# Kernel optimization log

Measured on AMD Instinct MI355X. Metric: run time of the kernel, lower is better.

Reference implementation:

```python
import jax, jax.numpy as jnp
import numpy as np
from math import sqrt

B, P, D = 4, 2048, 1024
H, DK = 16, 64  # n_heads, d_keys


def setup_inputs() -> dict:
    key = jax.random.key(0)
    ks = jax.random.split(key, 6)
    s = 1.0 / sqrt(D)
    return {
        "target_embedding": jax.random.normal(ks[0], (B, P, D), dtype=jnp.float32),
        "Wq": jax.random.normal(ks[1], (D, H * DK), dtype=jnp.float32) * s,
        "bq": jnp.zeros((H * DK,), dtype=jnp.float32),
        "Wk": jax.random.normal(ks[2], (D, H * DK), dtype=jnp.float32) * s,
        "bk": jnp.zeros((H * DK,), dtype=jnp.float32),
        "Wv": jax.random.normal(ks[3], (D, H * DK), dtype=jnp.float32) * s,
        "bv": jnp.zeros((H * DK,), dtype=jnp.float32),
        "Wo": jax.random.normal(ks[4], (H * DK, D), dtype=jnp.float32) * s,
        "bo": jnp.zeros((D,), dtype=jnp.float32),
    }


def reference(target_embedding, Wq, bq, Wk, bk, Wv, bv, Wo, bo):
    x = target_embedding
    b, p, _ = x.shape
    # QKV projections -> [B, P, H, DK]
    q = (x @ Wq + bq).reshape(b, p, H, DK)
    k = (x @ Wk + bk).reshape(b, p, H, DK)
    v = (x @ Wv + bv).reshape(b, p, H, DK)
    scale = 1.0 / sqrt(DK)
    scores = jnp.einsum("bphd,bqhd->bhpq", q, k)  # [B, H, P, P]
    A = jax.nn.softmax(scale * scores, axis=-1)  # dropout is identity in eval
    rep = jnp.einsum("bhpq,bqhd->bphd", A, v).reshape(b, p, H * DK)
    return rep @ Wo + bo
```

## Files before the change

### kernel.cpp

```cpp
#include <hip/hip_runtime.h>

typedef __attribute__((ext_vector_type(8))) short short8;
typedef __attribute__((ext_vector_type(4))) short short4v;
typedef __attribute__((ext_vector_type(4))) float f32x4;
typedef __attribute__((ext_vector_type(4))) unsigned short ushort4v;
typedef __attribute__((ext_vector_type(2))) unsigned int uint2v;

#define GLOBAL_AS __attribute__((address_space(1)))
#define LDS_AS    __attribute__((address_space(3)))

__device__ __forceinline__ unsigned short f2bf(float f) {
    unsigned int u = __float_as_uint(f);
    u += 0x7fffu + ((u >> 16) & 1u);
    return (unsigned short)(u >> 16);
}

__device__ __forceinline__ unsigned int pack_rhu(float a, float b) {
    unsigned int ua = __float_as_uint(a) + 0x8000u;
    unsigned int ub = __float_as_uint(b) + 0x8000u;
    return __builtin_amdgcn_perm(ub, ua, 0x07060302u);
}

__device__ __forceinline__ short4v pack4_rhu(float p0, float p1, float p2, float p3) {
    uint2v uu;
    uu[0] = pack_rhu(p0, p1);
    uu[1] = pack_rhu(p2, p3);
    return __builtin_bit_cast(short4v, uu);
}

__device__ __forceinline__ float fexp2(float x) {
    return __builtin_amdgcn_exp2f(x);
}

__device__ __forceinline__ void async_cp16(void* lds, const void* g) {
    __builtin_amdgcn_global_load_lds((GLOBAL_AS unsigned int*)g,
                                     (LDS_AS unsigned int*)lds, 16, 0, 0);
}

#define SCL2E 0.18033688011112042591999058512524f

__global__ void convert_x_kernel(const float* __restrict__ X,
                                 unsigned short* __restrict__ Xb) {
    int i = (blockIdx.x * 256 + threadIdx.x) * 4;
    float4 v = *(const float4*)&X[i];
    ushort4v o;
    o.x = f2bf(v.x); o.y = f2bf(v.y); o.z = f2bf(v.z); o.w = f2bf(v.w);
    *(ushort4v*)&Xb[i] = o;
}

__global__ void transpose_w_kernel(const float* __restrict__ Wq,
                                   const float* __restrict__ Wk,
                                   const float* __restrict__ Wv,
                                   const float* __restrict__ Wo,
                                   unsigned short* __restrict__ Wts) {
    __shared__ float tile[32][33];
    const int z = blockIdx.z;
    const float* src = (z == 0) ? Wq : (z == 1) ? Wk : (z == 2) ? Wv : Wo;
    unsigned short* dst = Wts + z * 1048576;
    const int tx = threadIdx.x, ty = threadIdx.y;
    const int x0 = blockIdx.x * 32, y0 = blockIdx.y * 32;
#pragma unroll
    for (int i = 0; i < 32; i += 8)
        tile[ty + i][tx] = src[(y0 + ty + i) * 1024 + x0 + tx];
    __syncthreads();
#pragma unroll
    for (int i = 0; i < 32; i += 8)
        dst[(x0 + ty + i) * 1024 + y0 + tx] = f2bf(tile[tx][ty + i]);
}

__global__ void transpose_v_kernel(const unsigned short* __restrict__ V,
                                   unsigned short* __restrict__ Vt) {
    __shared__ unsigned short tile[32][33];
    const int bh = blockIdx.z;
    const int p0 = blockIdx.x * 32, d0 = blockIdx.y * 32;
    const unsigned short* src = V + bh * (2048 * 64);
    unsigned short* dst = Vt + bh * (2048 * 64);
    const int tx = threadIdx.x, ty = threadIdx.y;
#pragma unroll
    for (int i = 0; i < 32; i += 8)
        tile[ty + i][tx] = src[(p0 + ty + i) * 64 + d0 + tx];
    __syncthreads();
#pragma unroll
    for (int i = 0; i < 32; i += 8)
        dst[(d0 + ty + i) * 2048 + p0 + tx] = tile[tx][ty + i];
}

__device__ __forceinline__ void gemm_mainloop_128(
    const unsigned short* __restrict__ A, const unsigned short* __restrict__ Bt,
    int m0, int n0, unsigned short* As, unsigned short* Bs, f32x4 acc[4][4]) {
    const int tid = threadIdx.x;
    const int lane = tid & 63;
    const int wave = tid >> 6;
    const int wr = wave >> 1, wc = wave & 1;
    const int c = lane & 15, quad = lane >> 4;

#pragma unroll
    for (int mt = 0; mt < 4; ++mt)
#pragma unroll
        for (int nt = 0; nt < 4; ++nt)
            acc[mt][nt] = (f32x4)0.0f;

    for (int k0 = 0; k0 < 1024; k0 += 32) {
#pragma unroll
        for (int i = 0; i < 2; ++i) {
            int s = tid + 256 * i;
            int r = s >> 2, gp = s & 3;
            int g = gp ^ ((r >> 1) & 3);
            async_cp16(&As[s * 8], &A[(m0 + r) * 1024 + k0 + g * 8]);
        }
#pragma unroll
        for (int i = 0; i < 2; ++i) {
            int s = tid + 256 * i;
            int r = s >> 2, gp = s & 3;
            int g = gp ^ ((r >> 1) & 3);
            async_cp16(&Bs[s * 8], &Bt[(n0 + r) * 1024 + k0 + g * 8]);
        }
        asm volatile("s_waitcnt vmcnt(0)" ::: "memory");
        __syncthreads();

        short8 af[4], bf[4];
#pragma unroll
        for (int mt = 0; mt < 4; ++mt) {
            int r = wr * 64 + mt * 16 + c;
            int gp = quad ^ ((r >> 1) & 3);
            af[mt] = *(const short8*)&As[r * 32 + gp * 8];
        }
#pragma unroll
        for (int nt = 0; nt < 4; ++nt) {
            int r = wc * 64 + nt * 16 + c;
            int gp = quad ^ ((r >> 1) & 3);
            bf[nt] = *(const short8*)&Bs[r * 32 + gp * 8];
        }
#pragma unroll
        for (int mt = 0; mt < 4; ++mt)
#pragma unroll
            for (int nt = 0; nt < 4; ++nt)
                acc[mt][nt] = __builtin_amdgcn_mfma_f32_16x16x32_bf16(
                    af[mt], bf[nt], acc[mt][nt], 0, 0, 0);
        __syncthreads();
    }
}

__global__ __launch_bounds__(256, 3) void gemm_qkv_kernel(
    const unsigned short* __restrict__ Xb, const unsigned short* __restrict__ Wts,
    const float* __restrict__ bq, const float* __restrict__ bk,
    const float* __restrict__ bv, unsigned short* __restrict__ Qb,
    unsigned short* __restrict__ Kb, unsigned short* __restrict__ Vb) {
    __shared__ __align__(16) unsigned short As[128 * 32];
    __shared__ __align__(16) unsigned short Bs[128 * 32];
    const int z = blockIdx.z;
    const unsigned short* Bt = Wts + z * 1048576;
    const float* bias = (z == 0) ? bq : (z == 1) ? bk : bv;
    const int m0 = blockIdx.y * 128, n0 = blockIdx.x * 128;
    f32x4 acc[4][4];
    gemm_mainloop_128(Xb, Bt, m0, n0, As, Bs, acc);

    const int lane = threadIdx.x & 63, wave = threadIdx.x >> 6;
    const int wr = wave >> 1, wc = wave & 1;
    const int c = lane & 15, quad = lane >> 4;
    unsigned short* dst = (z == 0) ? Qb : (z == 1) ? Kb : Vb;
    const float qscale = (z == 0) ? SCL2E : 1.0f;
#pragma unroll
    for (int nt = 0; nt < 4; ++nt) {
        int col = n0 + wc * 64 + nt * 16 + c;
        float bb = bias[col];
        int h = col >> 6, dk = col & 63;
#pragma unroll
        for (int mt = 0; mt < 4; ++mt) {
#pragma unroll
            for (int r = 0; r < 4; ++r) {
                int row = m0 + wr * 64 + mt * 16 + quad * 4 + r;
                int b = row >> 11, p = row & 2047;
                float v = (acc[mt][nt][r] + bb) * qscale;
                dst[((b * 16 + h) * 2048 + p) * 64 + dk] = f2bf(v);
            }
        }
    }
}

__device__ __forceinline__ void load_kv_regs(
    const unsigned short* __restrict__ Kbh, const unsigned short* __restrict__ Vbh,
    int k0, int tid, short8 kr[2], short8 vr[2]) {
#pragma unroll
    for (int i = 0; i < 2; ++i) {
        int s = tid + 256 * i;
        int r = s >> 3, gp = s & 7;
        int g = gp ^ (r & 7);
        kr[i] = *(const short8*)&Kbh[(k0 + r) * 64 + g * 8];
        vr[i] = *(const short8*)&Vbh[r * 2048 + k0 + g * 8];
    }
}

__global__ __launch_bounds__(256, 2) void attn_kernel(
    const unsigned short* __restrict__ Q, const unsigned short* __restrict__ K,
    const unsigned short* __restrict__ Vt, unsigned short* __restrict__ rep) {
    __shared__ __align__(16) unsigned short SMEM[16384];
    const int tid = threadIdx.x, lane = tid & 63, wave = tid >> 6;
    const int c = lane & 15, quad = lane >> 4;
    const int bh = blockIdx.y;
    const int q0 = blockIdx.x * 256 + wave * 64;
    const unsigned short* Qbh = Q + bh * (2048 * 64);
    const unsigned short* Kbh = K + bh * (2048 * 64);
    const unsigned short* Vbh = Vt + bh * (64 * 2048);

    short8 qf[4][2];
#pragma unroll
    for (int t = 0; t < 4; ++t)
#pragma unroll
        for (int ks = 0; ks < 2; ++ks)
            qf[t][ks] = *(const short8*)&Qbh[(q0 + t * 16 + c) * 64 + ks * 32 + quad * 8];

    short8 kr[2], vr[2];
    load_kv_regs(Kbh, Vbh, 0, tid, kr, vr);

    f32x4 o[4][4];
    float lpart[4] = {0.0f, 0.0f, 0.0f, 0.0f};
#pragma unroll
    for (int t = 0; t < 4; ++t)
#pragma unroll
        for (int d = 0; d < 4; ++d) o[t][d] = (f32x4)0.0f;

    for (int it = 0; it < 32; ++it) {
        const int buf = it & 1;
        unsigned short* Ksb = &SMEM[buf * 4096];
        unsigned short* Vsb = &SMEM[8192 + buf * 4096];
#pragma unroll
        for (int i = 0; i < 2; ++i) {
            int s = tid + 256 * i;
            *(short8*)&Ksb[s * 8] = kr[i];
            *(short8*)&Vsb[s * 8] = vr[i];
        }
        __syncthreads();
        if (it < 31)
            load_kv_regs(Kbh, Vbh, (it + 1) * 64, tid, kr, vr);

        short8 kf[4][2];
#pragma unroll
        for (int nt = 0; nt < 4; ++nt)
#pragma unroll
            for (int ks = 0; ks < 2; ++ks) {
                int r = nt * 16 + c;
                int gp2 = (quad + 4 * ks) ^ (r & 7);
                kf[nt][ks] = *(const short8*)&Ksb[r * 64 + gp2 * 8];
            }

        short4v pfrag[4][4];
#pragma unroll
        for (int t = 0; t < 4; ++t) {
#pragma unroll
            for (int nt = 0; nt < 4; ++nt) {
                f32x4 z4 = (f32x4)0.0f;
                z4 = __builtin_amdgcn_mfma_f32_16x16x32_bf16(kf[nt][0], qf[t][0], z4, 0, 0, 0);
                z4 = __builtin_amdgcn_mfma_f32_16x16x32_bf16(kf[nt][1], qf[t][1], z4, 0, 0, 0);
                float p0 = fexp2(z4[0]), p1 = fexp2(z4[1]);
                float p2 = fexp2(z4[2]), p3 = fexp2(z4[3]);
                lpart[t] += (p0 + p1) + (p2 + p3);
                pfrag[nt][t] = pack4_rhu(p0, p1, p2, p3);
            }
        }

#pragma unroll
        for (int dkt = 0; dkt < 4; ++dkt) {
            int r = dkt * 16 + c;
#pragma unroll
            for (int kt = 0; kt < 4; ++kt) {
                int gbase = 2 * kt + (quad >> 1);
                int g = gbase ^ (r & 7);
                int eloff = g * 8 + (quad & 1) * 4;
                short4v vf4 = *(const short4v*)&Vsb[r * 64 + eloff];
#pragma unroll
                for (int t = 0; t < 4; ++t)
                    o[t][dkt] = __builtin_amdgcn_mfma_f32_16x16x16bf16_1k(
                        vf4, pfrag[kt][t], o[t][dkt], 0, 0, 0);
            }
        }
    }

    float inv[4];
#pragma unroll
    for (int t = 0; t < 4; ++t) {
        float l = lpart[t];
        l += __shfl_xor(l, 16);
        l += __shfl_xor(l, 32);
        inv[t] = 1.0f / l;
    }

    __syncthreads();
    const int b = bh >> 4, h = bh & 15;
    unsigned short* ob = &SMEM[wave * 2304];
#pragma unroll
    for (int pass = 0; pass < 2; ++pass) {
#pragma unroll
        for (int th = 0; th < 2; ++th) {
            int t = pass * 2 + th;
#pragma unroll
            for (int dkt = 0; dkt < 4; ++dkt) {
                short4v frag = pack4_rhu(o[t][dkt][0] * inv[t], o[t][dkt][1] * inv[t],
                                         o[t][dkt][2] * inv[t], o[t][dkt][3] * inv[t]);
                *(short4v*)&ob[(th * 16 + c) * 72 + dkt * 16 + quad * 4] = frag;
            }
        }
        asm volatile("s_waitcnt lgkmcnt(0)" ::: "memory");
#pragma unroll
        for (int sp = 0; sp < 4; ++sp) {
            int qr = sp * 8 + (lane >> 3);
            int d8 = (lane & 7) * 8;
            short8 row = *(const short8*)&ob[qr * 72 + d8];
            *(short8*)&rep[(b * 2048 + q0 + pass * 32 + qr) * 1024 + h * 64 + d8] = row;
        }
    }
}

__global__ __launch_bounds__(256, 3) void gemm_out_kernel(
    const unsigned short* __restrict__ rep, const unsigned short* __restrict__ Wot,
    const float* __restrict__ bo, float* __restrict__ out) {
    __shared__ __align__(16) unsigned short As[128 * 32];
    __shared__ __align__(16) unsigned short Bs[128 * 32];
    const int m0 = blockIdx.y * 128, n0 = blockIdx.x * 128;
    f32x4 acc[4][4];
    gemm_mainloop_128(rep, Wot, m0, n0, As, Bs, acc);
    const int lane = threadIdx.x & 63, wave = threadIdx.x >> 6;
    const int wr = wave >> 1, wc = wave & 1;
    const int c = lane & 15, quad = lane >> 4;
#pragma unroll
    for (int nt = 0; nt < 4; ++nt) {
        int col = n0 + wc * 64 + nt * 16 + c;
        float bb = bo[col];
#pragma unroll
        for (int mt = 0; mt < 4; ++mt) {
            int row = m0 + wr * 64 + mt * 16 + quad * 4;
#pragma unroll
            for (int r = 0; r < 4; ++r)
                out[(row + r) * 1024 + col] = acc[mt][nt][r] + bb;
        }
    }
}

extern "C" void kernel_launch(void* const* d_in, const int* in_sizes, int n_in,
                              void* d_out, int out_size, void* d_ws, size_t ws_size,
                              hipStream_t stream) {
    (void)in_sizes; (void)n_in; (void)out_size; (void)ws_size;
    const float* X  = (const float*)d_in[0];
    const float* Wq = (const float*)d_in[1];
    const float* bq = (const float*)d_in[2];
    const float* Wk = (const float*)d_in[3];
    const float* bk = (const float*)d_in[4];
    const float* Wv = (const float*)d_in[5];
    const float* bv = (const float*)d_in[6];
    const float* Wo = (const float*)d_in[7];
    const float* bo = (const float*)d_in[8];
    float* out = (float*)d_out;

    char* ws = (char*)d_ws;
    unsigned short* Xb   = (unsigned short*)(ws);
    unsigned short* Wts  = (unsigned short*)(ws + (16u << 20));
    unsigned short* Qb   = (unsigned short*)(ws + (24u << 20));
    unsigned short* Kb   = (unsigned short*)(ws + (40u << 20));
    unsigned short* Vb   = (unsigned short*)(ws + (56u << 20));
    unsigned short* Vtb  = (unsigned short*)(ws);
    unsigned short* repb = (unsigned short*)(ws + (56u << 20));

    convert_x_kernel<<<8192, 256, 0, stream>>>(X, Xb);
    transpose_w_kernel<<<dim3(32, 32, 4), dim3(32, 8), 0, stream>>>(Wq, Wk, Wv, Wo, Wts);
    gemm_qkv_kernel<<<dim3(8, 64, 3), 256, 0, stream>>>(Xb, Wts, bq, bk, bv, Qb, Kb, Vb);
    transpose_v_kernel<<<dim3(64, 2, 64), dim3(32, 8), 0, stream>>>(Vb, Vtb);
    attn_kernel<<<dim3(8, 64), 256, 0, stream>>>(Qb, Kb, Vtb, repb);
    gemm_out_kernel<<<dim3(8, 64), 256, 0, stream>>>(repb, Wts + 3 * 1048576, bo, out);
}
```

Before: 310.0 us.

## Fuse prep kernels, write V transposed from QKV GEMM, read K/V directly in attention

Merges the X conversion and weight transpose into one launch. The QKV GEMM epilogue now stages V through shared memory and writes it already transposed, which removes the separate V transpose kernel. The attention kernel drops its LDS double-buffered K/V staging and block barriers and loads fragments straight from global memory (relying on L2), with a remapped block index that groups heads. Direct global loads avoid barrier cost but may raise memory latency and duplicate traffic across waves.

Result: slower. 383.2 us (+23.6%).

```diff
diff --git a/kernel.cpp b/kernel.cpp
--- a/kernel.cpp
+++ b/kernel.cpp
@@ -39,50 +39,40 @@
 
 #define SCL2E 0.18033688011112042591999058512524f
 
-__global__ void convert_x_kernel(const float* __restrict__ X,
-                                 unsigned short* __restrict__ Xb) {
-    int i = (blockIdx.x * 256 + threadIdx.x) * 4;
-    float4 v = *(const float4*)&X[i];
-    ushort4v o;
-    o.x = f2bf(v.x); o.y = f2bf(v.y); o.z = f2bf(v.z); o.w = f2bf(v.w);
-    *(ushort4v*)&Xb[i] = o;
-}
-
-__global__ void transpose_w_kernel(const float* __restrict__ Wq,
-                                   const float* __restrict__ Wk,
-                                   const float* __restrict__ Wv,
-                                   const float* __restrict__ Wo,
-                                   unsigned short* __restrict__ Wts) {
-    __shared__ float tile[32][33];
+__global__ void prep_kernel(const float* __restrict__ X,
+                            const float* __restrict__ Wq,
+                            const float* __restrict__ Wk,
+                            const float* __restrict__ Wv,
+                            const float* __restrict__ Wo,
+                            unsigned short* __restrict__ Xb,
+                            unsigned short* __restrict__ Wts) {
     const int z = blockIdx.z;
-    const float* src = (z == 0) ? Wq : (z == 1) ? Wk : (z == 2) ? Wv : Wo;
-    unsigned short* dst = Wts + z * 1048576;
-    const int tx = threadIdx.x, ty = threadIdx.y;
-    const int x0 = blockIdx.x * 32, y0 = blockIdx.y * 32;
-#pragma unroll
-    for (int i = 0; i < 32; i += 8)
-        tile[ty + i][tx] = src[(y0 + ty + i) * 1024 + x0 + tx];
-    __syncthreads();
-#pragma unroll
-    for (int i = 0; i < 32; i += 8)
-        dst[(x0 + ty + i) * 1024 + y0 + tx] = f2bf(tile[tx][ty + i]);
-}
-
-__global__ void transpose_v_kernel(const unsigned short* __restrict__ V,
-                                   unsigned short* __restrict__ Vt) {
-    __shared__ unsigned short tile[32][33];
-    const int bh = blockIdx.z;
-    const int p0 = blockIdx.x * 32, d0 = blockIdx.y * 32;
-    const unsigned short* src = V + bh * (2048 * 64);
-    unsigned short* dst = Vt + bh * (2048 * 64);
-    const int tx = threadIdx.x, ty = threadIdx.y;
-#pragma unroll
-    for (int i = 0; i < 32; i += 8)
-        tile[ty + i][tx] = src[(p0 + ty + i) * 64 + d0 + tx];
-    __syncthreads();
-#pragma unroll
-    for (int i = 0; i < 32; i += 8)
-        dst[(d0 + ty + i) * 2048 + p0 + tx] = tile[tx][ty + i];
+    if (z < 4) {
+        __shared__ float tile[32][33];
+        const float* src = (z == 0) ? Wq : (z == 1) ? Wk : (z == 2) ? Wv : Wo;
+        unsigned short* dst = Wts + z * 1048576;
+        const int tx = threadIdx.x, ty = threadIdx.y;
+        const int x0 = blockIdx.x * 32, y0 = blockIdx.y * 32;
+#pragma unroll
+        for (int i = 0; i < 32; i += 8)
+            tile[ty + i][tx] = src[(y0 + ty + i) * 1024 + x0 + tx];
+        __syncthreads();
+#pragma unroll
+        for (int i = 0; i < 32; i += 8)
+            dst[(x0 + ty + i) * 1024 + y0 + tx] = f2bf(tile[tx][ty + i]);
+    } else {
+        const int tid = threadIdx.y * 32 + threadIdx.x;
+        const int chunk = blockIdx.y * 32 + blockIdx.x;
+        const int base = chunk * 8192;
+#pragma unroll
+        for (int pass = 0; pass < 8; ++pass) {
+            int i = base + pass * 1024 + tid * 4;
+            float4 v = *(const float4*)&X[i];
+            ushort4v o;
+            o.x = f2bf(v.x); o.y = f2bf(v.y); o.z = f2bf(v.z); o.w = f2bf(v.w);
+            *(ushort4v*)&Xb[i] = o;
+        }
+    }
 }
 
 __device__ __forceinline__ void gemm_mainloop_128(
@@ -145,9 +135,10 @@
     const unsigned short* __restrict__ Xb, const unsigned short* __restrict__ Wts,
     const float* __restrict__ bq, const float* __restrict__ bk,
     const float* __restrict__ bv, unsigned short* __restrict__ Qb,
-    unsigned short* __restrict__ Kb, unsigned short* __restrict__ Vb) {
-    __shared__ __align__(16) unsigned short As[128 * 32];
-    __shared__ __align__(16) unsigned short Bs[128 * 32];
+    unsigned short* __restrict__ Kb, unsigned short* __restrict__ Vtb) {
+    __shared__ __align__(16) unsigned short SH[17408];
+    unsigned short* As = SH;
+    unsigned short* Bs = SH + 4096;
     const int z = blockIdx.z;
     const unsigned short* Bt = Wts + z * 1048576;
     const float* bias = (z == 0) ? bq : (z == 1) ? bk : bv;
@@ -155,50 +146,66 @@
     f32x4 acc[4][4];
     gemm_mainloop_128(Xb, Bt, m0, n0, As, Bs, acc);
 
-    const int lane = threadIdx.x & 63, wave = threadIdx.x >> 6;
+    const int tid = threadIdx.x;
+    const int lane = tid & 63, wave = tid >> 6;
     const int wr = wave >> 1, wc = wave & 1;
     const int c = lane & 15, quad = lane >> 4;
-    unsigned short* dst = (z == 0) ? Qb : (z == 1) ? Kb : Vb;
-    const float qscale = (z == 0) ? SCL2E : 1.0f;
-#pragma unroll
-    for (int nt = 0; nt < 4; ++nt) {
-        int col = n0 + wc * 64 + nt * 16 + c;
-        float bb = bias[col];
-        int h = col >> 6, dk = col & 63;
-#pragma unroll
-        for (int mt = 0; mt < 4; ++mt) {
-#pragma unroll
-            for (int r = 0; r < 4; ++r) {
-                int row = m0 + wr * 64 + mt * 16 + quad * 4 + r;
-                int b = row >> 11, p = row & 2047;
-                float v = (acc[mt][nt][r] + bb) * qscale;
-                dst[((b * 16 + h) * 2048 + p) * 64 + dk] = f2bf(v);
-            }
-        }
-    }
-}
-
-__device__ __forceinline__ void load_kv_regs(
-    const unsigned short* __restrict__ Kbh, const unsigned short* __restrict__ Vbh,
-    int k0, int tid, short8 kr[2], short8 vr[2]) {
-#pragma unroll
-    for (int i = 0; i < 2; ++i) {
-        int s = tid + 256 * i;
-        int r = s >> 3, gp = s & 7;
-        int g = gp ^ (r & 7);
-        kr[i] = *(const short8*)&Kbh[(k0 + r) * 64 + g * 8];
-        vr[i] = *(const short8*)&Vbh[r * 2048 + k0 + g * 8];
+    const int b = m0 >> 11, p0 = m0 & 2047;
+
+    if (z < 2) {
+        unsigned short* dst = (z == 0) ? Qb : Kb;
+        const float qscale = (z == 0) ? SCL2E : 1.0f;
+#pragma unroll
+        for (int nt = 0; nt < 4; ++nt) {
+            int col = n0 + wc * 64 + nt * 16 + c;
+            float bb = bias[col];
+            int h = col >> 6, dk = col & 63;
+#pragma unroll
+            for (int mt = 0; mt < 4; ++mt) {
+#pragma unroll
+                for (int r = 0; r < 4; ++r) {
+                    int p = p0 + wr * 64 + mt * 16 + quad * 4 + r;
+                    float v = (acc[mt][nt][r] + bb) * qscale;
+                    dst[((b * 16 + h) * 2048 + p) * 64 + dk] = f2bf(v);
+                }
+            }
+        }
+    } else {
+#pragma unroll
+        for (int nt = 0; nt < 4; ++nt) {
+            int col = wc * 64 + nt * 16 + c;
+            float bb = bias[n0 + col];
+#pragma unroll
+            for (int mt = 0; mt < 4; ++mt) {
+                int p = wr * 64 + mt * 16 + quad * 4;
+                short4v v = pack4_rhu(acc[mt][nt][0] + bb, acc[mt][nt][1] + bb,
+                                      acc[mt][nt][2] + bb, acc[mt][nt][3] + bb);
+                *(short4v*)&SH[col * 136 + p] = v;
+            }
+        }
+        __syncthreads();
+#pragma unroll
+        for (int pass = 0; pass < 8; ++pass) {
+            int col = pass * 16 + (tid >> 4);
+            int gcol = n0 + col;
+            int h = gcol >> 6, dk = gcol & 63;
+            int p8 = (tid & 15) * 8;
+            short8 row = *(const short8*)&SH[col * 136 + p8];
+            *(short8*)&Vtb[((b * 16 + h) * 64 + dk) * 2048 + p0 + p8] = row;
+        }
     }
 }
 
 __global__ __launch_bounds__(256, 2) void attn_kernel(
     const unsigned short* __restrict__ Q, const unsigned short* __restrict__ K,
     const unsigned short* __restrict__ Vt, unsigned short* __restrict__ rep) {
-    __shared__ __align__(16) unsigned short SMEM[16384];
+    __shared__ __align__(16) unsigned short ob[4][2304];
     const int tid = threadIdx.x, lane = tid & 63, wave = tid >> 6;
     const int c = lane & 15, quad = lane >> 4;
-    const int bh = blockIdx.y;
-    const int q0 = blockIdx.x * 256 + wave * 64;
+    const int id = blockIdx.x;
+    const int bh = (id & 7) * 8 + ((id >> 3) & 7);
+    const int qblk = id >> 6;
+    const int q0 = qblk * 256 + wave * 64;
     const unsigned short* Qbh = Q + bh * (2048 * 64);
     const unsigned short* Kbh = K + bh * (2048 * 64);
     const unsigned short* Vbh = Vt + bh * (64 * 2048);
@@ -210,9 +217,6 @@
         for (int ks = 0; ks < 2; ++ks)
             qf[t][ks] = *(const short8*)&Qbh[(q0 + t * 16 + c) * 64 + ks * 32 + quad * 8];
 
-    short8 kr[2], vr[2];
-    load_kv_regs(Kbh, Vbh, 0, tid, kr, vr);
-
     f32x4 o[4][4];
     float lpart[4] = {0.0f, 0.0f, 0.0f, 0.0f};
 #pragma unroll
@@ -220,29 +224,15 @@
 #pragma unroll
         for (int d = 0; d < 4; ++d) o[t][d] = (f32x4)0.0f;
 
+#pragma unroll 2
     for (int it = 0; it < 32; ++it) {
-        const int buf = it & 1;
-        unsigned short* Ksb = &SMEM[buf * 4096];
-        unsigned short* Vsb = &SMEM[8192 + buf * 4096];
-#pragma unroll
-        for (int i = 0; i < 2; ++i) {
-            int s = tid + 256 * i;
-            *(short8*)&Ksb[s * 8] = kr[i];
-            *(short8*)&Vsb[s * 8] = vr[i];
-        }
-        __syncthreads();
-        if (it < 31)
-            load_kv_regs(Kbh, Vbh, (it + 1) * 64, tid, kr, vr);
-
+        const int k0 = it * 64;
         short8 kf[4][2];
 #pragma unroll
         for (int nt = 0; nt < 4; ++nt)
 #pragma unroll
-            for (int ks = 0; ks < 2; ++ks) {
-                int r = nt * 16 + c;
-                int gp2 = (quad + 4 * ks) ^ (r & 7);
-                kf[nt][ks] = *(const short8*)&Ksb[r * 64 + gp2 * 8];
-            }
+            for (int ks = 0; ks < 2; ++ks)
+                kf[nt][ks] = *(const short8*)&Kbh[(k0 + nt * 16 + c) * 64 + ks * 32 + quad * 8];
 
         short4v pfrag[4][4];
 #pragma unroll
@@ -261,13 +251,10 @@
 
 #pragma unroll
         for (int dkt = 0; dkt < 4; ++dkt) {
-            int r = dkt * 16 + c;
+            const unsigned short* vrow = &Vbh[(dkt * 16 + c) * 2048 + k0 + quad * 4];
 #pragma unroll
             for (int kt = 0; kt < 4; ++kt) {
-                int gbase = 2 * kt + (quad >> 1);
-                int g = gbase ^ (r & 7);
-                int eloff = g * 8 + (quad & 1) * 4;
-                short4v vf4 = *(const short4v*)&Vsb[r * 64 + eloff];
+                short4v vf4 = *(const short4v*)&vrow[kt * 16];
 #pragma unroll
                 for (int t = 0; t < 4; ++t)
                     o[t][dkt] = __builtin_amdgcn_mfma_f32_16x16x16bf16_1k(
@@ -285,9 +272,8 @@
         inv[t] = 1.0f / l;
     }
 
-    __syncthreads();
     const int b = bh >> 4, h = bh & 15;
-    unsigned short* ob = &SMEM[wave * 2304];
+    unsigned short* obw = ob[wave];
 #pragma unroll
     for (int pass = 0; pass < 2; ++pass) {
 #pragma unroll
@@ -297,7 +283,7 @@
             for (int dkt = 0; dkt < 4; ++dkt) {
                 short4v frag = pack4_rhu(o[t][dkt][0] * inv[t], o[t][dkt][1] * inv[t],
                                          o[t][dkt][2] * inv[t], o[t][dkt][3] * inv[t]);
-                *(short4v*)&ob[(th * 16 + c) * 72 + dkt * 16 + quad * 4] = frag;
+                *(short4v*)&obw[(th * 16 + c) * 72 + dkt * 16 + quad * 4] = frag;
             }
         }
         asm volatile("s_waitcnt lgkmcnt(0)" ::: "memory");
@@ -305,7 +291,7 @@
         for (int sp = 0; sp < 4; ++sp) {
             int qr = sp * 8 + (lane >> 3);
             int d8 = (lane & 7) * 8;
-            short8 row = *(const short8*)&ob[qr * 72 + d8];
+            short8 row = *(const short8*)&obw[qr * 72 + d8];
             *(short8*)&rep[(b * 2048 + q0 + pass * 32 + qr) * 1024 + h * 64 + d8] = row;
         }
     }
@@ -356,14 +342,11 @@
     unsigned short* Wts  = (unsigned short*)(ws + (16u << 20));
     unsigned short* Qb   = (unsigned short*)(ws + (24u << 20));
     unsigned short* Kb   = (unsigned short*)(ws + (40u << 20));
-    unsigned short* Vb   = (unsigned short*)(ws + (56u << 20));
-    unsigned short* Vtb  = (unsigned short*)(ws);
-    unsigned short* repb = (unsigned short*)(ws + (56u << 20));
-
-    convert_x_kernel<<<8192, 256, 0, stream>>>(X, Xb);
-    transpose_w_kernel<<<dim3(32, 32, 4), dim3(32, 8), 0, stream>>>(Wq, Wk, Wv, Wo, Wts);
-    gemm_qkv_kernel<<<dim3(8, 64, 3), 256, 0, stream>>>(Xb, Wts, bq, bk, bv, Qb, Kb, Vb);
-    transpose_v_kernel<<<dim3(64, 2, 64), dim3(32, 8), 0, stream>>>(Vb, Vtb);
-    attn_kernel<<<dim3(8, 64), 256, 0, stream>>>(Qb, Kb, Vtb, repb);
+    unsigned short* Vtb  = (unsigned short*)(ws + (56u << 20));
+    unsigned short* repb = (unsigned short*)(ws);
+
+    prep_kernel<<<dim3(32, 32, 5), dim3(32, 8), 0, stream>>>(X, Wq, Wk, Wv, Wo, Xb, Wts);
+    gemm_qkv_kernel<<<dim3(8, 64, 3), 256, 0, stream>>>(Xb, Wts, bq, bk, bv, Qb, Kb, Vtb);
+    attn_kernel<<<512, 256, 0, stream>>>(Qb, Kb, Vtb, repb);
     gemm_out_kernel<<<dim3(8, 64), 256, 0, stream>>>(repb, Wts + 3 * 1048576, bo, out);
 }
```
